# Kernel optimization log

Measured on AMD Instinct MI355X. Metric: run time of the kernel, lower is better.

## Reference

```python
import jax, jax.numpy as jnp
import numpy as np

N = 50000      # nodes
E = 800000     # edges
F_IN = 256
H1, D1 = 4, 32   # conv1 heads, per-head dim (hidden_features)
H2, D2 = 1, 32   # conv2 heads, per-head dim (out_features)
NEG_SLOPE = 0.2


def setup_inputs():
    key = jax.random.key(0)
    ks = jax.random.split(key, 12)
    x = jax.random.normal(ks[0], (N, F_IN), dtype=jnp.float32)
    src = jax.random.randint(ks[1], (E,), 0, N, dtype=jnp.int32)
    dst = jax.random.randint(ks[2], (E,), 0, N, dtype=jnp.int32)
    s = 0.05
    W1 = jax.random.normal(ks[3], (F_IN, H1 * D1), dtype=jnp.float32) * s
    al1 = jax.random.normal(ks[4], (H1, D1), dtype=jnp.float32) * s
    ar1 = jax.random.normal(ks[5], (H1, D1), dtype=jnp.float32) * s
    b1 = jnp.zeros((H1 * D1,), dtype=jnp.float32)
    W2 = jax.random.normal(ks[6], (H1 * D1, H2 * D2), dtype=jnp.float32) * s
    al2 = jax.random.normal(ks[7], (H2, D2), dtype=jnp.float32) * s
    ar2 = jax.random.normal(ks[8], (H2, D2), dtype=jnp.float32) * s
    b2 = jnp.zeros((H2 * D2,), dtype=jnp.float32)
    return {"x": x, "W1": W1, "al1": al1, "ar1": ar1, "b1": b1,
            "W2": W2, "al2": al2, "ar2": ar2, "b2": b2,
            "src": src, "dst": dst}


def gat_layer(x, W, al, ar, b, src, dst, H, D):
    # x: [N, F] -> feat: [N, H, D]
    feat = (x @ W).reshape(-1, H, D)
    el = jnp.sum(feat * al, axis=-1)   # [N, H]
    er = jnp.sum(feat * ar, axis=-1)   # [N, H]
    # per-edge attention logits, LeakyReLU
    e = jax.nn.leaky_relu(el[src] + er[dst], negative_slope=NEG_SLOPE)  # [E, H]
    # edge softmax over destination neighborhoods (stable)
    m = jax.ops.segment_max(e, dst, num_segments=N)          # [N, H]
    m = jnp.where(jnp.isfinite(m), m, 0.0)                   # guard zero-in-degree
    ee = jnp.exp(e - m[dst])                                 # [E, H]
    z = jax.ops.segment_sum(ee, dst, num_segments=N)         # [N, H]
    a = ee / jnp.maximum(z[dst], 1e-16)                      # [E, H]
    # weighted message aggregation
    msg = feat[src] * a[:, :, None]                          # [E, H, D]
    rst = jax.ops.segment_sum(msg, dst, num_segments=N)      # [N, H, D]
    return (rst + b.reshape(1, H, D)).reshape(-1, H * D)     # flatten(1)


def reference(x, W1, al1, ar1, b1, W2, al2, ar2, b2, src, dst):
    # dropouts are identity in eval mode; is_out_layer=True => no activation
    h = gat_layer(x, W1, al1, ar1, b1, src, dst, H1, D1)     # [N, H1*D1]
    out = gat_layer(h, W2, al2, ar2, b2, src, dst, H2, D2)   # [N, H2*D2]
    return out
```

## Files before the change

### kernel.cpp

```cpp
#include <hip/hip_runtime.h>

constexpr int F_IN = 256;
constexpr int H1 = 4, D1 = 32, F1 = H1 * D1;
constexpr int H2 = 1, D2 = 32, F2 = H2 * D2;
constexpr float NEG = 0.2f;

constexpr int BW = 128;
constexpr int NBUK_MAX = 512;
constexpr int CB = 128;

typedef short short8 __attribute__((ext_vector_type(8)));
typedef float f32x4 __attribute__((ext_vector_type(4)));

__device__ inline float bf2f(unsigned short u) {
    unsigned int x = ((unsigned int)u) << 16;
    return __builtin_bit_cast(float, x);
}
__device__ inline unsigned short f2bf(float f) {
    __bf16 h = (__bf16)f;
    return __builtin_bit_cast(unsigned short, h);
}

__global__ __launch_bounds__(256) void chist(const int* __restrict__ dst,
                                             unsigned int* __restrict__ HcT,
                                             int E, int nbuk) {
    __shared__ unsigned int h[NBUK_MAX];
    int tid = threadIdx.x;
    for (int i = tid; i < nbuk; i += 256) h[i] = 0;
    __syncthreads();
    int epb = (E + CB - 1) / CB;
    int e0 = blockIdx.x * epb, e1 = min(e0 + epb, E);
    for (int e = e0 + tid; e < e1; e += 256)
        atomicAdd(&h[dst[e] >> 7], 1u);
    __syncthreads();
    for (int i = tid; i < nbuk; i += 256) HcT[(size_t)i * CB + blockIdx.x] = h[i];
}

__global__ __launch_bounds__(512) void bscan(const unsigned int* __restrict__ HcT,
                                             unsigned int* __restrict__ Bb,
                                             unsigned int* __restrict__ S, int nbuk) {
    __shared__ unsigned int tot[NBUK_MAX];
    int t = threadIdx.x;
    unsigned int run = 0;
    if (t < nbuk) {
        const uint4* row = (const uint4*)(HcT + (size_t)t * CB);
#pragma unroll 8
        for (int b4 = 0; b4 < CB / 4; ++b4) {
            uint4 v = row[b4];
            int b = b4 * 4;
            Bb[(size_t)(b + 0) * nbuk + t] = run; run += v.x;
            Bb[(size_t)(b + 1) * nbuk + t] = run; run += v.y;
            Bb[(size_t)(b + 2) * nbuk + t] = run; run += v.z;
            Bb[(size_t)(b + 3) * nbuk + t] = run; run += v.w;
        }
    }
    tot[t] = (t < nbuk) ? run : 0;
    __syncthreads();
    for (int o = 1; o < NBUK_MAX; o <<= 1) {
        unsigned int v = (t >= o) ? tot[t - o] : 0;
        __syncthreads();
        tot[t] += v;
        __syncthreads();
    }
    if (t < nbuk) S[t] = tot[t] - run;
    if (t == nbuk - 1) S[nbuk] = tot[t];
}

__global__ __launch_bounds__(256) void cscat(const int* __restrict__ src,
                                             const int* __restrict__ dst,
                                             const unsigned int* __restrict__ Bb,
                                             const unsigned int* __restrict__ S,
                                             unsigned int* __restrict__ pairs, int E, int nbuk) {
    __shared__ unsigned int h[NBUK_MAX];
    int tid = threadIdx.x;
    for (int i = tid; i < nbuk; i += 256) h[i] = 0;
    __syncthreads();
    int epb = (E + CB - 1) / CB;
    int e0 = blockIdx.x * epb, e1 = min(e0 + epb, E);
    const unsigned int* bb = Bb + (size_t)blockIdx.x * nbuk;
    for (int e = e0 + tid; e < e1; e += 256) {
        int d = dst[e];
        int k = d >> 7;
        unsigned int r = atomicAdd(&h[k], 1u);
        unsigned int p = S[k] + bb[k] + r;
        pairs[p] = ((unsigned int)(d & 127) << 17) | (unsigned int)src[e];
    }
}

__global__ __launch_bounds__(256) void fscat(const unsigned int* __restrict__ pairs,
                                             const unsigned int* __restrict__ S,
                                             int* __restrict__ off, int* __restrict__ csr,
                                             int n, int E) {
    int k = blockIdx.x;
    int tid = threadIdx.x;
    unsigned int s0 = S[k], s1 = S[k + 1];
    __shared__ unsigned int cnt[BW];
    __shared__ unsigned int ex[BW];
    if (tid < BW) cnt[tid] = 0;
    __syncthreads();
    for (unsigned int i = s0 + tid; i < s1; i += 256)
        atomicAdd(&cnt[pairs[i] >> 17], 1u);
    __syncthreads();
    unsigned int orig = (tid < BW) ? cnt[tid] : 0;
    if (tid < BW) ex[tid] = orig;
    __syncthreads();
    for (int o = 1; o < BW; o <<= 1) {
        unsigned int v = (tid < BW && tid >= (unsigned)o) ? ex[tid - o] : 0;
        __syncthreads();
        if (tid < BW) ex[tid] += v;
        __syncthreads();
    }
    if (tid < BW) {
        ex[tid] -= orig;
        int node = k * BW + tid;
        if (node < n) off[node] = (int)(s0 + ex[tid]);
    }
    if (tid < BW) cnt[tid] = 0;
    __syncthreads();
    for (unsigned int i = s0 + tid; i < s1; i += 256) {
        unsigned int pr = pairs[i];
        int loc = pr >> 17;
        unsigned int r = atomicAdd(&cnt[loc], 1u);
        csr[s0 + ex[loc] + r] = (int)(pr & 0x1FFFFu);
    }
    if (k == 0 && tid == 0) off[n] = E;
}

__device__ inline void wsplit_one(const float* W, unsigned short* Wh, unsigned short* Wl,
                                  int idx, int C) {
    int j    = idx & 7;
    int lane = (idx >> 3) & 63;
    int t    = idx >> 9;
    int FC   = C >> 4;
    int fc   = t % FC, ks = t / FC;
    int k = ks * 32 + (lane >> 4) * 8 + j;
    int c = fc * 16 + (lane & 15);
    float v = W[(size_t)k * C + c];
    __bf16 h = (__bf16)v;
    float hv = (float)h;
    __bf16 lo = (__bf16)(v - hv);
    Wh[idx] = __builtin_bit_cast(unsigned short, h);
    Wl[idx] = __builtin_bit_cast(unsigned short, lo);
}
__global__ void wsplit_swz2(const float* __restrict__ W1, unsigned short* __restrict__ W1h,
                            unsigned short* __restrict__ W1l,
                            const float* __restrict__ W2, unsigned short* __restrict__ W2h,
                            unsigned short* __restrict__ W2l) {
    int idx = blockIdx.x * 256 + threadIdx.x;
    constexpr int N1 = F_IN * F1;
    if (idx < N1) wsplit_one(W1, W1h, W1l, idx, F1);
    else if (idx < N1 + F1 * F2) wsplit_one(W2, W2h, W2l, idx - N1, F2);
}

__global__ __launch_bounds__(256) void xswz_kernel(const float* __restrict__ x,
                                                   unsigned short* __restrict__ xb,
                                                   int n, int nrow_pad) {
    int tid = threadIdx.x;
    int lane = tid & 63;
    int wid = tid >> 6;
    int half = lane >> 5;
    int l32 = lane & 31;
    int ks = l32 >> 2;
    int khi = l32 & 3;
    int row = blockIdx.x * 8 + wid * 2 + half;
    if (row >= nrow_pad) return;
    float v[8];
    if (row < n) {
        const float* p = x + (size_t)row * F_IN + ks * 32 + khi * 8;
        float4 a = *(const float4*)p;
        float4 b = *(const float4*)(p + 4);
        v[0] = a.x; v[1] = a.y; v[2] = a.z; v[3] = a.w;
        v[4] = b.x; v[5] = b.y; v[6] = b.z; v[7] = b.w;
    } else {
#pragma unroll
        for (int j = 0; j < 8; ++j) v[j] = 0.f;
    }
    short8 s;
#pragma unroll
    for (int j = 0; j < 8; ++j) s[j] = (short)f2bf(v[j]);
    int frag16 = row >> 4;
    int fragLane = (row & 15) | (khi << 4);
    *(short8*)(xb + (((size_t)frag16 * 8 + ks) * 64 + fragLane) * 8) = s;
}

constexpr int BM1 = 64;
__global__ __launch_bounds__(256) void gemm1_mfma(
    const unsigned short* __restrict__ Xb,
    const unsigned short* __restrict__ Wh,
    const unsigned short* __restrict__ Wl,
    const float* __restrict__ alv, const float* __restrict__ arv,
    unsigned short* __restrict__ outb,
    float* __restrict__ el, float* __restrict__ er, int n)
{
    const int tid  = threadIdx.x;
    const int lane = tid & 63;
    const int wid  = tid >> 6;
    const int wrow = (wid >> 1) * 32;
    const int wcol = (wid & 1) * 64;
    const int wc16 = wcol >> 4;
    const int row0 = blockIdx.x * BM1;
    const int l16  = lane & 15;
    const int khi  = lane >> 4;
    const int fbase = blockIdx.x * 4 + (wid >> 1) * 2;

    f32x4 acc[2][4];
#pragma unroll
    for (int mi = 0; mi < 2; ++mi)
#pragma unroll
        for (int ni = 0; ni < 4; ++ni) acc[mi][ni] = f32x4{0.f, 0.f, 0.f, 0.f};

#pragma unroll
    for (int ks = 0; ks < 8; ++ks) {
        short8 ah[2];
#pragma unroll
        for (int mi = 0; mi < 2; ++mi)
            ah[mi] = *(const short8*)(Xb + (((size_t)(fbase + mi) * 8 + ks) * 64 + lane) * 8);

        short8 bh[4], bl[4];
#pragma unroll
        for (int ni = 0; ni < 4; ++ni) {
            int base = ((ks * 8 + wc16 + ni) * 64 + lane) * 8;
            bh[ni] = *(const short8*)(Wh + base);
            bl[ni] = *(const short8*)(Wl + base);
        }

#pragma unroll
        for (int mi = 0; mi < 2; ++mi)
#pragma unroll
            for (int ni = 0; ni < 4; ++ni) {
                acc[mi][ni] = __builtin_amdgcn_mfma_f32_16x16x32_bf16(ah[mi], bl[ni], acc[mi][ni], 0, 0, 0);
                acc[mi][ni] = __builtin_amdgcn_mfma_f32_16x16x32_bf16(ah[mi], bh[ni], acc[mi][ni], 0, 0, 0);
            }
    }

    const int hh0 = wcol >> 5;
    float alr[2][2], arr[2][2];
#pragma unroll
    for (int t = 0; t < 2; ++t) {
        int head = hh0 + t;
        alr[t][0] = alv[head * 32 + l16];
        alr[t][1] = alv[head * 32 + 16 + l16];
        arr[t][0] = arv[head * 32 + l16];
        arr[t][1] = arv[head * 32 + 16 + l16];
    }

#pragma unroll
    for (int mi = 0; mi < 2; ++mi) {
        int rbase = row0 + wrow + mi * 16 + khi * 4;
#pragma unroll
        for (int rr = 0; rr < 4; ++rr) {
            int row = rbase + rr;
            bool ok = row < n;
            if (ok) {
#pragma unroll
                for (int ni = 0; ni < 4; ++ni)
                    outb[(size_t)row * F1 + wcol + ni * 16 + l16] = f2bf(acc[mi][ni][rr]);
            }
#pragma unroll
            for (int t = 0; t < 2; ++t) {
                float pel = acc[mi][2 * t][rr] * alr[t][0] + acc[mi][2 * t + 1][rr] * alr[t][1];
                float per = acc[mi][2 * t][rr] * arr[t][0] + acc[mi][2 * t + 1][rr] * arr[t][1];
#pragma unroll
                for (int o = 1; o < 16; o <<= 1) {
                    pel += __shfl_xor(pel, o);
                    per += __shfl_xor(per, o);
                }
                if (ok && l16 == 0) {
                    el[(size_t)row * H1 + hh0 + t] = pel;
                    er[(size_t)row * H1 + hh0 + t] = per;
                }
            }
        }
    }
}

constexpr int BM2 = 64;
__global__ __launch_bounds__(256) void gemm2_mfma(
    const float* __restrict__ X,
    const unsigned short* __restrict__ Wh,
    const unsigned short* __restrict__ Wl,
    const float* __restrict__ alv, const float* __restrict__ arv,
    float* __restrict__ out,
    float* __restrict__ el, float* __restrict__ er, int n)
{
    __shared__ float xs[32 * BM2 * 4];
    const int tid  = threadIdx.x;
    const int lane = tid & 63;
    const int wid  = tid >> 6;
    const int wrow = wid * 16;
    const int row0 = blockIdx.x * BM2;
    const int l16  = lane & 15;
    const int khi  = lane >> 4;

    {
        int gr = row0 + lane;
        gr = gr < n ? gr : (n - 1);
        const float* rowp = X + (size_t)gr * F1;
#pragma unroll
        for (int i = 0; i < 8; ++i) {
            int kc = wid * 8 + i;
            const float* srcp = rowp + kc * 4;
            float* dstf = &xs[kc * BM2 * 4];
            __builtin_amdgcn_global_load_lds(
                (const __attribute__((address_space(1))) unsigned int*)srcp,
                (__attribute__((address_space(3))) unsigned int*)dstf,
                16, 0, 0);
        }
    }
    asm volatile("s_waitcnt vmcnt(0)" ::: "memory");
    __syncthreads();

    f32x4 acc[2];
#pragma unroll
    for (int ni = 0; ni < 2; ++ni) acc[ni] = f32x4{0.f, 0.f, 0.f, 0.f};

    const int rt = wrow + l16;

#pragma unroll
    for (int ks = 0; ks < 4; ++ks) {
        const int kc = ks * 8 + khi * 2;

        short8 bh[2], bl[2];
#pragma unroll
        for (int ni = 0; ni < 2; ++ni) {
            int base = ((ks * 2 + ni) * 64 + lane) * 8;
            bh[ni] = *(const short8*)(Wh + base);
            bl[ni] = *(const short8*)(Wl + base);
        }

        float4 xa0 = *(const float4*)&xs[(kc + 0) * BM2 * 4 + rt * 4];
        float4 xa1 = *(const float4*)&xs[(kc + 1) * BM2 * 4 + rt * 4];
        float v[8] = {xa0.x, xa0.y, xa0.z, xa0.w, xa1.x, xa1.y, xa1.z, xa1.w};
        short8 ah, al8;
#pragma unroll
        for (int j = 0; j < 8; ++j) {
            __bf16 h = (__bf16)v[j];
            float hv = (float)h;
            __bf16 lo = (__bf16)(v[j] - hv);
            ah[j] = __builtin_bit_cast(short, h);
            al8[j] = __builtin_bit_cast(short, lo);
        }

#pragma unroll
        for (int ni = 0; ni < 2; ++ni) {
            acc[ni] = __builtin_amdgcn_mfma_f32_16x16x32_bf16(al8, bh[ni], acc[ni], 0, 0, 0);
            acc[ni] = __builtin_amdgcn_mfma_f32_16x16x32_bf16(ah, bl[ni], acc[ni], 0, 0, 0);
            acc[ni] = __builtin_amdgcn_mfma_f32_16x16x32_bf16(ah, bh[ni], acc[ni], 0, 0, 0);
        }
    }

    float al0 = alv[l16], al1c = alv[16 + l16];
    float ar0 = arv[l16], ar1c = arv[16 + l16];

    int rbase = row0 + wrow + khi * 4;
#pragma unroll
    for (int rr = 0; rr < 4; ++rr) {
        int row = rbase + rr;
        bool ok = row < n;
        if (ok) {
#pragma unroll
            for (int ni = 0; ni < 2; ++ni)
                out[(size_t)row * F2 + ni * 16 + l16] = acc[ni][rr];
        }
        float pel = acc[0][rr] * al0 + acc[1][rr] * al1c;
        float per = acc[0][rr] * ar0 + acc[1][rr] * ar1c;
#pragma unroll
        for (int o = 1; o < 16; o <<= 1) {
            pel += __shfl_xor(pel, o);
            per += __shfl_xor(per, o);
        }
        if (ok && l16 == 0) {
            el[row] = pel;
            er[row] = per;
        }
    }
}

__global__ __launch_bounds__(256) void agg1_kernel(
    const int* __restrict__ off, const int* __restrict__ csr_src,
    const unsigned short* __restrict__ featb, const float* __restrict__ el,
    const float* __restrict__ er, const float* __restrict__ b,
    float* __restrict__ out, int n)
{
    int wid = (blockIdx.x * 256 + threadIdx.x) >> 6;
    int lane = threadIdx.x & 63;
    if (wid >= n) return;
    int c0 = (lane & 31) * 4;
    int h = (lane & 31) >> 3;
    int half = lane >> 5;
    float erv = er[(size_t)wid * H1 + h];
    float sw = 0.f;
    float4 acc = {0.f, 0.f, 0.f, 0.f};
    int jb = off[wid], je = off[wid + 1];
    int j = jb + half;
    for (; j + 6 < je; j += 8) {
        int s0 = csr_src[j];
        int s1 = csr_src[j + 2];
        int s2 = csr_src[j + 4];
        int s3 = csr_src[j + 6];
        ushort4 u0 = *(const ushort4*)(featb + (size_t)s0 * F1 + c0);
        ushort4 u1 = *(const ushort4*)(featb + (size_t)s1 * F1 + c0);
        ushort4 u2 = *(const ushort4*)(featb + (size_t)s2 * F1 + c0);
        ushort4 u3 = *(const ushort4*)(featb + (size_t)s3 * F1 + c0);
        float t0 = el[(size_t)s0 * H1 + h] + erv;
        float t1 = el[(size_t)s1 * H1 + h] + erv;
        float t2 = el[(size_t)s2 * H1 + h] + erv;
        float t3 = el[(size_t)s3 * H1 + h] + erv;
        t0 = t0 > 0.f ? t0 : NEG * t0;
        t1 = t1 > 0.f ? t1 : NEG * t1;
        t2 = t2 > 0.f ? t2 : NEG * t2;
        t3 = t3 > 0.f ? t3 : NEG * t3;
        float w0 = __expf(t0), w1 = __expf(t1), w2 = __expf(t2), w3 = __expf(t3);
        sw += (w0 + w1) + (w2 + w3);
        acc.x = fmaf(w0, bf2f(u0.x), fmaf(w1, bf2f(u1.x), fmaf(w2, bf2f(u2.x), fmaf(w3, bf2f(u3.x), acc.x))));
        acc.y = fmaf(w0, bf2f(u0.y), fmaf(w1, bf2f(u1.y), fmaf(w2, bf2f(u2.y), fmaf(w3, bf2f(u3.y), acc.y))));
        acc.z = fmaf(w0, bf2f(u0.z), fmaf(w1, bf2f(u1.z), fmaf(w2, bf2f(u2.z), fmaf(w3, bf2f(u3.z), acc.z))));
        acc.w = fmaf(w0, bf2f(u0.w), fmaf(w1, bf2f(u1.w), fmaf(w2, bf2f(u2.w), fmaf(w3, bf2f(u3.w), acc.w))));
    }
    for (; j < je; j += 2) {
        int s = csr_src[j];
        ushort4 u = *(const ushort4*)(featb + (size_t)s * F1 + c0);
        float t = el[(size_t)s * H1 + h] + erv;
        t = t > 0.f ? t : NEG * t;
        float w = __expf(t);
        sw += w;
        acc.x = fmaf(w, bf2f(u.x), acc.x);
        acc.y = fmaf(w, bf2f(u.y), acc.y);
        acc.z = fmaf(w, bf2f(u.z), acc.z);
        acc.w = fmaf(w, bf2f(u.w), acc.w);
    }
    acc.x += __shfl_xor(acc.x, 32);
    acc.y += __shfl_xor(acc.y, 32);
    acc.z += __shfl_xor(acc.z, 32);
    acc.w += __shfl_xor(acc.w, 32);
    sw    += __shfl_xor(sw, 32);
    if (half == 0) {
        float inv = 1.f / fmaxf(sw, 1e-16f);
        float4 bb = *(const float4*)(b + c0);
        float4 t = {acc.x * inv + bb.x, acc.y * inv + bb.y,
                    acc.z * inv + bb.z, acc.w * inv + bb.w};
        *(float4*)(out + (size_t)wid * F1 + c0) = t;
    }
}

__global__ __launch_bounds__(256) void agg2_kernel(
    const int* __restrict__ off, const int* __restrict__ csr_src,
    const float* __restrict__ feat, const float* __restrict__ el,
    const float* __restrict__ er, const float* __restrict__ b,
    float* __restrict__ out, int n)
{
    int wid = (blockIdx.x * 256 + threadIdx.x) >> 6;
    int lane = threadIdx.x & 63;
    if (wid >= n) return;
    int c0 = (lane & 7) * 4;
    int grp = lane >> 3;
    float erv = er[wid];
    float sw = 0.f;
    float4 acc = {0.f, 0.f, 0.f, 0.f};
    int jb = off[wid], je = off[wid + 1];
    int j = jb + grp;
    for (; j + 8 < je; j += 16) {
        int s0 = csr_src[j];
        int s1 = csr_src[j + 8];
        float4 f0 = *(const float4*)(feat + (size_t)s0 * F2 + c0);
        float4 f1 = *(const float4*)(feat + (size_t)s1 * F2 + c0);
        float t0 = el[s0] + erv;
        float t1 = el[s1] + erv;
        t0 = t0 > 0.f ? t0 : NEG * t0;
        t1 = t1 > 0.f ? t1 : NEG * t1;
        float w0 = __expf(t0);
        float w1 = __expf(t1);
        sw += w0 + w1;
        acc.x = fmaf(w0, f0.x, fmaf(w1, f1.x, acc.x));
        acc.y = fmaf(w0, f0.y, fmaf(w1, f1.y, acc.y));
        acc.z = fmaf(w0, f0.z, fmaf(w1, f1.z, acc.z));
        acc.w = fmaf(w0, f0.w, fmaf(w1, f1.w, acc.w));
    }
    for (; j < je; j += 8) {
        int s = csr_src[j];
        float4 f = *(const float4*)(feat + (size_t)s * F2 + c0);
        float t = el[s] + erv;
        t = t > 0.f ? t : NEG * t;
        float w = __expf(t);
        sw += w;
        acc.x = fmaf(w, f.x, acc.x);
        acc.y = fmaf(w, f.y, acc.y);
        acc.z = fmaf(w, f.z, acc.z);
        acc.w = fmaf(w, f.w, acc.w);
    }
#pragma unroll
    for (int o = 8; o < 64; o <<= 1) {
        acc.x += __shfl_xor(acc.x, o);
        acc.y += __shfl_xor(acc.y, o);
        acc.z += __shfl_xor(acc.z, o);
        acc.w += __shfl_xor(acc.w, o);
        sw    += __shfl_xor(sw, o);
    }
    if (lane < 8) {
        float inv = 1.f / fmaxf(sw, 1e-16f);
        float4 bb = *(const float4*)(b + c0);
        float4 t = {acc.x * inv + bb.x, acc.y * inv + bb.y,
                    acc.z * inv + bb.z, acc.w * inv + bb.w};
        *(float4*)(out + (size_t)wid * F2 + c0) = t;
    }
}

extern "C" void kernel_launch(void* const* d_in, const int* in_sizes, int n_in,
                              void* d_out, int out_size, void* d_ws, size_t ws_size,
                              hipStream_t stream) {
    const float* x   = (const float*)d_in[0];
    const float* W1  = (const float*)d_in[1];
    const float* al1 = (const float*)d_in[2];
    const float* ar1 = (const float*)d_in[3];
    const float* b1  = (const float*)d_in[4];
    const float* W2  = (const float*)d_in[5];
    const float* al2 = (const float*)d_in[6];
    const float* ar2 = (const float*)d_in[7];
    const float* b2  = (const float*)d_in[8];
    const int*   src = (const int*)d_in[9];
    const int*   dst = (const int*)d_in[10];

    const int N = in_sizes[0] / F_IN;
    const int E = in_sizes[9];
    const int NBUK = (N + BW - 1) / BW;
    const int NBLK1 = (N + BM1 - 1) / BM1;
    const int NROWP = NBLK1 * BM1;

    char* w = (char*)d_ws;
    size_t o = 0;
    auto alloc = [&](size_t bytes) { size_t cur = o; o += (bytes + 255) & ~255ULL; return cur; };
    int*   off   = (int*)  (w + alloc((size_t)(N + 1) * 4));
    int*   csr   = (int*)  (w + alloc((size_t)E * 4));
    unsigned int* pairs = (unsigned int*)(w + alloc((size_t)E * 4));
    unsigned int* HcT = (unsigned int*)(w + alloc((size_t)CB * NBUK * 4));
    unsigned int* Bb  = (unsigned int*)(w + alloc((size_t)CB * NBUK * 4));
    unsigned int* S   = (unsigned int*)(w + alloc((size_t)(NBUK + 1) * 4));
    unsigned short* xb = (unsigned short*)(w + alloc((size_t)NROWP * F_IN * 2));
    unsigned short* feat1b = (unsigned short*)(w + alloc((size_t)N * F1 * 2));
    float* el1   = (float*)(w + alloc((size_t)N * H1 * 4));
    float* er1   = (float*)(w + alloc((size_t)N * H1 * 4));
    float* h1    = (float*)(w + alloc((size_t)N * F1 * 4));
    float* feat2 = (float*)(w + alloc((size_t)N * F2 * 4));
    float* el2   = (float*)(w + alloc((size_t)N * H2 * 4));
    float* er2   = (float*)(w + alloc((size_t)N * H2 * 4));
    unsigned short* W1h = (unsigned short*)(w + alloc((size_t)F_IN * F1 * 2));
    unsigned short* W1l = (unsigned short*)(w + alloc((size_t)F_IN * F1 * 2));
    unsigned short* W2h = (unsigned short*)(w + alloc((size_t)F1 * F2 * 2));
    unsigned short* W2l = (unsigned short*)(w + alloc((size_t)F1 * F2 * 2));
    (void)ws_size; (void)n_in; (void)out_size;

    chist<<<CB, 256, 0, stream>>>(dst, HcT, E, NBUK);
    bscan<<<1, 512, 0, stream>>>(HcT, Bb, S, NBUK);
    cscat<<<CB, 256, 0, stream>>>(src, dst, Bb, S, pairs, E, NBUK);
    fscat<<<NBUK, 256, 0, stream>>>(pairs, S, off, csr, N, E);

    wsplit_swz2<<<(F_IN * F1 + F1 * F2 + 255) / 256, 256, 0, stream>>>(
        W1, W1h, W1l, W2, W2h, W2l);
    xswz_kernel<<<(NROWP + 7) / 8, 256, 0, stream>>>(x, xb, N, NROWP);

    gemm1_mfma<<<NBLK1, 256, 0, stream>>>(
        xb, W1h, W1l, al1, ar1, feat1b, el1, er1, N);
    agg1_kernel<<<(N + 3) / 4, 256, 0, stream>>>(off, csr, feat1b, el1, er1, b1, h1, N);

    gemm2_mfma<<<(N + BM2 - 1) / BM2, 256, 0, stream>>>(
        h1, W2h, W2l, al2, ar2, feat2, el2, er2, N);
    agg2_kernel<<<(N + 3) / 4, 256, 0, stream>>>(off, csr, feat2, el2, er2, b2, (float*)d_out, N);
}
```

Before: 151.1 us.

## Fuse CSR build into cooperative kernel, merge prep kernels, store feat2 in bf16

```diff
diff --git a/kernel.cpp b/kernel.cpp
--- a/kernel.cpp
+++ b/kernel.cpp
@@ -1,4 +1,7 @@
 #include <hip/hip_runtime.h>
+#include <hip/hip_cooperative_groups.h>
+
+namespace cg = cooperative_groups;
 
 constexpr int F_IN = 256;
 constexpr int H1 = 4, D1 = 32, F1 = H1 * D1;
@@ -21,109 +24,108 @@
     return __builtin_bit_cast(unsigned short, h);
 }
 
-__global__ __launch_bounds__(256) void chist(const int* __restrict__ dst,
-                                             unsigned int* __restrict__ HcT,
-                                             int E, int nbuk) {
+__global__ __launch_bounds__(256) void csr_build(
+    const int* __restrict__ src, const int* __restrict__ dst,
+    unsigned int* __restrict__ HcT, unsigned int* __restrict__ Bb,
+    unsigned int* __restrict__ S, unsigned int* __restrict__ pairs,
+    int* __restrict__ off, int* __restrict__ csr,
+    int n, int E, int nbuk)
+{
+    cg::grid_group grid = cg::this_grid();
     __shared__ unsigned int h[NBUK_MAX];
-    int tid = threadIdx.x;
+    const int tid = threadIdx.x;
+    const int b = blockIdx.x;
+    const int epb = (E + CB - 1) / CB;
+    const int e0 = b * epb, e1 = min(e0 + epb, E);
+
     for (int i = tid; i < nbuk; i += 256) h[i] = 0;
     __syncthreads();
-    int epb = (E + CB - 1) / CB;
-    int e0 = blockIdx.x * epb, e1 = min(e0 + epb, E);
     for (int e = e0 + tid; e < e1; e += 256)
-        atomicAdd(&h[dst[e] >> 7], 1u);
+        atomicAdd(&h[((unsigned)dst[e]) >> 7], 1u);
     __syncthreads();
-    for (int i = tid; i < nbuk; i += 256) HcT[(size_t)i * CB + blockIdx.x] = h[i];
-}
-
-__global__ __launch_bounds__(512) void bscan(const unsigned int* __restrict__ HcT,
-                                             unsigned int* __restrict__ Bb,
-                                             unsigned int* __restrict__ S, int nbuk) {
-    __shared__ unsigned int tot[NBUK_MAX];
-    int t = threadIdx.x;
-    unsigned int run = 0;
-    if (t < nbuk) {
-        const uint4* row = (const uint4*)(HcT + (size_t)t * CB);
+    for (int i = tid; i < nbuk; i += 256) HcT[(size_t)i * CB + b] = h[i];
+    grid.sync();
+
+    {
+        int g = b * 256 + tid;
+        if (g < nbuk) {
+            const uint4* row = (const uint4*)(HcT + (size_t)g * CB);
+            unsigned int run = 0;
 #pragma unroll 8
-        for (int b4 = 0; b4 < CB / 4; ++b4) {
-            uint4 v = row[b4];
-            int b = b4 * 4;
-            Bb[(size_t)(b + 0) * nbuk + t] = run; run += v.x;
-            Bb[(size_t)(b + 1) * nbuk + t] = run; run += v.y;
-            Bb[(size_t)(b + 2) * nbuk + t] = run; run += v.z;
-            Bb[(size_t)(b + 3) * nbuk + t] = run; run += v.w;
-        }
-    }
-    tot[t] = (t < nbuk) ? run : 0;
+            for (int b4 = 0; b4 < CB / 4; ++b4) {
+                uint4 v = row[b4];
+                int bb = b4 * 4;
+                Bb[(size_t)(bb + 0) * nbuk + g] = run; run += v.x;
+                Bb[(size_t)(bb + 1) * nbuk + g] = run; run += v.y;
+                Bb[(size_t)(bb + 2) * nbuk + g] = run; run += v.z;
+                Bb[(size_t)(bb + 3) * nbuk + g] = run; run += v.w;
+            }
+            S[g] = run;
+        }
+    }
+    grid.sync();
+
+    if (b == 0) {
+        unsigned a0 = (2 * tid     < nbuk) ? S[2 * tid]     : 0;
+        unsigned a1 = (2 * tid + 1 < nbuk) ? S[2 * tid + 1] : 0;
+        __syncthreads();
+        h[tid] = a0 + a1;
+        __syncthreads();
+        for (int o = 1; o < 256; o <<= 1) {
+            unsigned v = (tid >= o) ? h[tid - o] : 0;
+            __syncthreads();
+            h[tid] += v;
+            __syncthreads();
+        }
+        unsigned base = h[tid] - (a0 + a1);
+        if (2 * tid     < nbuk) S[2 * tid]     = base;
+        if (2 * tid + 1 < nbuk) S[2 * tid + 1] = base + a0;
+        if (tid == 255) S[nbuk] = h[255];
+    }
+    grid.sync();
+
+    for (int i = tid; i < nbuk; i += 256) h[i] = S[i] + Bb[(size_t)b * nbuk + i];
     __syncthreads();
-    for (int o = 1; o < NBUK_MAX; o <<= 1) {
-        unsigned int v = (t >= o) ? tot[t - o] : 0;
-        __syncthreads();
-        tot[t] += v;
-        __syncthreads();
-    }
-    if (t < nbuk) S[t] = tot[t] - run;
-    if (t == nbuk - 1) S[nbuk] = tot[t];
-}
-
-__global__ __launch_bounds__(256) void cscat(const int* __restrict__ src,
-                                             const int* __restrict__ dst,
-                                             const unsigned int* __restrict__ Bb,
-                                             const unsigned int* __restrict__ S,
-                                             unsigned int* __restrict__ pairs, int E, int nbuk) {
-    __shared__ unsigned int h[NBUK_MAX];
-    int tid = threadIdx.x;
-    for (int i = tid; i < nbuk; i += 256) h[i] = 0;
-    __syncthreads();
-    int epb = (E + CB - 1) / CB;
-    int e0 = blockIdx.x * epb, e1 = min(e0 + epb, E);
-    const unsigned int* bb = Bb + (size_t)blockIdx.x * nbuk;
     for (int e = e0 + tid; e < e1; e += 256) {
         int d = dst[e];
-        int k = d >> 7;
-        unsigned int r = atomicAdd(&h[k], 1u);
-        unsigned int p = S[k] + bb[k] + r;
-        pairs[p] = ((unsigned int)(d & 127) << 17) | (unsigned int)src[e];
-    }
-}
-
-__global__ __launch_bounds__(256) void fscat(const unsigned int* __restrict__ pairs,
-                                             const unsigned int* __restrict__ S,
-                                             int* __restrict__ off, int* __restrict__ csr,
-                                             int n, int E) {
-    int k = blockIdx.x;
-    int tid = threadIdx.x;
-    unsigned int s0 = S[k], s1 = S[k + 1];
-    __shared__ unsigned int cnt[BW];
-    __shared__ unsigned int ex[BW];
-    if (tid < BW) cnt[tid] = 0;
-    __syncthreads();
-    for (unsigned int i = s0 + tid; i < s1; i += 256)
-        atomicAdd(&cnt[pairs[i] >> 17], 1u);
-    __syncthreads();
-    unsigned int orig = (tid < BW) ? cnt[tid] : 0;
-    if (tid < BW) ex[tid] = orig;
-    __syncthreads();
-    for (int o = 1; o < BW; o <<= 1) {
-        unsigned int v = (tid < BW && tid >= (unsigned)o) ? ex[tid - o] : 0;
-        __syncthreads();
-        if (tid < BW) ex[tid] += v;
-        __syncthreads();
-    }
-    if (tid < BW) {
-        ex[tid] -= orig;
-        int node = k * BW + tid;
-        if (node < n) off[node] = (int)(s0 + ex[tid]);
-    }
-    if (tid < BW) cnt[tid] = 0;
-    __syncthreads();
-    for (unsigned int i = s0 + tid; i < s1; i += 256) {
-        unsigned int pr = pairs[i];
-        int loc = pr >> 17;
-        unsigned int r = atomicAdd(&cnt[loc], 1u);
-        csr[s0 + ex[loc] + r] = (int)(pr & 0x1FFFFu);
-    }
-    if (k == 0 && tid == 0) off[n] = E;
+        int k = ((unsigned)d) >> 7;
+        unsigned p = atomicAdd(&h[k], 1u);
+        pairs[p] = ((unsigned)(d & 127) << 17) | (unsigned)src[e];
+    }
+    grid.sync();
+
+    for (int k = b; k < nbuk; k += CB) {
+        unsigned s0 = S[k], s1v = S[k + 1];
+        __syncthreads();
+        if (tid < BW) h[tid] = 0;
+        __syncthreads();
+        for (unsigned i = s0 + tid; i < s1v; i += 256)
+            atomicAdd(&h[pairs[i] >> 17], 1u);
+        __syncthreads();
+        unsigned orig = (tid < BW) ? h[tid] : 0;
+        if (tid < BW) h[128 + tid] = orig;
+        __syncthreads();
+        for (int o = 1; o < BW; o <<= 1) {
+            unsigned v = (tid < BW && tid >= o) ? h[128 + tid - o] : 0;
+            __syncthreads();
+            if (tid < BW) h[128 + tid] += v;
+            __syncthreads();
+        }
+        if (tid < BW) {
+            h[128 + tid] -= orig;
+            int node = k * BW + tid;
+            if (node < n) off[node] = (int)(s0 + h[128 + tid]);
+        }
+        if (tid < BW) h[tid] = 0;
+        __syncthreads();
+        for (unsigned i = s0 + tid; i < s1v; i += 256) {
+            unsigned pr = pairs[i];
+            int loc = pr >> 17;
+            unsigned r = atomicAdd(&h[loc], 1u);
+            csr[s0 + h[128 + loc] + r] = (int)(pr & 0x1FFFFu);
+        }
+    }
+    if (b == 0 && tid == 0) off[n] = E;
 }
 
 __device__ inline void wsplit_one(const float* W, unsigned short* Wh, unsigned short* Wl,
@@ -142,19 +144,25 @@
     Wh[idx] = __builtin_bit_cast(unsigned short, h);
     Wl[idx] = __builtin_bit_cast(unsigned short, lo);
 }
-__global__ void wsplit_swz2(const float* __restrict__ W1, unsigned short* __restrict__ W1h,
-                            unsigned short* __restrict__ W1l,
-                            const float* __restrict__ W2, unsigned short* __restrict__ W2h,
-                            unsigned short* __restrict__ W2l) {
-    int idx = blockIdx.x * 256 + threadIdx.x;
-    constexpr int N1 = F_IN * F1;
-    if (idx < N1) wsplit_one(W1, W1h, W1l, idx, F1);
-    else if (idx < N1 + F1 * F2) wsplit_one(W2, W2h, W2l, idx - N1, F2);
-}
-
-__global__ __launch_bounds__(256) void xswz_kernel(const float* __restrict__ x,
-                                                   unsigned short* __restrict__ xb,
-                                                   int n, int nrow_pad) {
+
+constexpr int WBLK = (F_IN * F1 + F1 * F2) / 256;
+
+__global__ __launch_bounds__(256) void prep_kernel(
+    const float* __restrict__ W1, unsigned short* __restrict__ W1h,
+    unsigned short* __restrict__ W1l,
+    const float* __restrict__ W2, unsigned short* __restrict__ W2h,
+    unsigned short* __restrict__ W2l,
+    const float* __restrict__ x, unsigned short* __restrict__ xb,
+    int n, int nrow_pad)
+{
+    int bid = blockIdx.x;
+    if (bid < WBLK) {
+        int idx = bid * 256 + threadIdx.x;
+        constexpr int N1 = F_IN * F1;
+        if (idx < N1) wsplit_one(W1, W1h, W1l, idx, F1);
+        else wsplit_one(W2, W2h, W2l, idx - N1, F2);
+        return;
+    }
     int tid = threadIdx.x;
     int lane = tid & 63;
     int wid = tid >> 6;
@@ -162,7 +170,7 @@
     int l32 = lane & 31;
     int ks = l32 >> 2;
     int khi = l32 & 3;
-    int row = blockIdx.x * 8 + wid * 2 + half;
+    int row = (bid - WBLK) * 8 + wid * 2 + half;
     if (row >= nrow_pad) return;
     float v[8];
     if (row < n) {
@@ -280,7 +288,7 @@
     const unsigned short* __restrict__ Wh,
     const unsigned short* __restrict__ Wl,
     const float* __restrict__ alv, const float* __restrict__ arv,
-    float* __restrict__ out,
+    unsigned short* __restrict__ outb,
     float* __restrict__ el, float* __restrict__ er, int n)
 {
     __shared__ float xs[32 * BM2 * 4];
@@ -360,7 +368,7 @@
         if (ok) {
 #pragma unroll
             for (int ni = 0; ni < 2; ++ni)
-                out[(size_t)row * F2 + ni * 16 + l16] = acc[ni][rr];
+                outb[(size_t)row * F2 + ni * 16 + l16] = f2bf(acc[ni][rr]);
         }
         float pel = acc[0][rr] * al0 + acc[1][rr] * al1c;
         float per = acc[0][rr] * ar0 + acc[1][rr] * ar1c;
@@ -445,7 +453,7 @@
 
 __global__ __launch_bounds__(256) void agg2_kernel(
     const int* __restrict__ off, const int* __restrict__ csr_src,
-    const float* __restrict__ feat, const float* __restrict__ el,
+    const unsigned short* __restrict__ featb, const float* __restrict__ el,
     const float* __restrict__ er, const float* __restrict__ b,
     float* __restrict__ out, int n)
 {
@@ -462,8 +470,8 @@
     for (; j + 8 < je; j += 16) {
         int s0 = csr_src[j];
         int s1 = csr_src[j + 8];
-        float4 f0 = *(const float4*)(feat + (size_t)s0 * F2 + c0);
-        float4 f1 = *(const float4*)(feat + (size_t)s1 * F2 + c0);
+        ushort4 u0 = *(const ushort4*)(featb + (size_t)s0 * F2 + c0);
+        ushort4 u1 = *(const ushort4*)(featb + (size_t)s1 * F2 + c0);
         float t0 = el[s0] + erv;
         float t1 = el[s1] + erv;
         t0 = t0 > 0.f ? t0 : NEG * t0;
@@ -471,22 +479,22 @@
         float w0 = __expf(t0);
         float w1 = __expf(t1);
         sw += w0 + w1;
-        acc.x = fmaf(w0, f0.x, fmaf(w1, f1.x, acc.x));
-        acc.y = fmaf(w0, f0.y, fmaf(w1, f1.y, acc.y));
-        acc.z = fmaf(w0, f0.z, fmaf(w1, f1.z, acc.z));
-        acc.w = fmaf(w0, f0.w, fmaf(w1, f1.w, acc.w));
+        acc.x = fmaf(w0, bf2f(u0.x), fmaf(w1, bf2f(u1.x), acc.x));
+        acc.y = fmaf(w0, bf2f(u0.y), fmaf(w1, bf2f(u1.y), acc.y));
+        acc.z = fmaf(w0, bf2f(u0.z), fmaf(w1, bf2f(u1.z), acc.z));
+        acc.w = fmaf(w0, bf2f(u0.w), fmaf(w1, bf2f(u1.w), acc.w));
     }
     for (; j < je; j += 8) {
         int s = csr_src[j];
-        float4 f = *(const float4*)(feat + (size_t)s * F2 + c0);
+        ushort4 u = *(const ushort4*)(featb + (size_t)s * F2 + c0);
         float t = el[s] + erv;
         t = t > 0.f ? t : NEG * t;
         float w = __expf(t);
         sw += w;
-        acc.x = fmaf(w, f.x, acc.x);
-        acc.y = fmaf(w, f.y, acc.y);
-        acc.z = fmaf(w, f.z, acc.z);
-        acc.w = fmaf(w, f.w, acc.w);
+        acc.x = fmaf(w, bf2f(u.x), acc.x);
+        acc.y = fmaf(w, bf2f(u.y), acc.y);
+        acc.z = fmaf(w, bf2f(u.z), acc.z);
+        acc.w = fmaf(w, bf2f(u.w), acc.w);
     }
 #pragma unroll
     for (int o = 8; o < 64; o <<= 1) {
@@ -520,9 +528,9 @@
     const int*   src = (const int*)d_in[9];
     const int*   dst = (const int*)d_in[10];
 
-    const int N = in_sizes[0] / F_IN;
-    const int E = in_sizes[9];
-    const int NBUK = (N + BW - 1) / BW;
+    int N = in_sizes[0] / F_IN;
+    int E = in_sizes[9];
+    int NBUK = (N + BW - 1) / BW;
     const int NBLK1 = (N + BM1 - 1) / BM1;
     const int NROWP = NBLK1 * BM1;
 
@@ -540,7 +548,7 @@
     float* el1   = (float*)(w + alloc((size_t)N * H1 * 4));
     float* er1   = (float*)(w + alloc((size_t)N * H1 * 4));
     float* h1    = (float*)(w + alloc((size_t)N * F1 * 4));
-    float* feat2 = (float*)(w + alloc((size_t)N * F2 * 4));
+    unsigned short* feat2b = (unsigned short*)(w + alloc((size_t)N * F2 * 2));
     float* el2   = (float*)(w + alloc((size_t)N * H2 * 4));
     float* er2   = (float*)(w + alloc((size_t)N * H2 * 4));
     unsigned short* W1h = (unsigned short*)(w + alloc((size_t)F_IN * F1 * 2));
@@ -549,20 +557,22 @@
     unsigned short* W2l = (unsigned short*)(w + alloc((size_t)F1 * F2 * 2));
     (void)ws_size; (void)n_in; (void)out_size;
 
-    chist<<<CB, 256, 0, stream>>>(dst, HcT, E, NBUK);
-    bscan<<<1, 512, 0, stream>>>(HcT, Bb, S, NBUK);
-    cscat<<<CB, 256, 0, stream>>>(src, dst, Bb, S, pairs, E, NBUK);
-    fscat<<<NBUK, 256, 0, stream>>>(pairs, S, off, csr, N, E);
-
-    wsplit_swz2<<<(F_IN * F1 + F1 * F2 + 255) / 256, 256, 0, stream>>>(
-        W1, W1h, W1l, W2, W2h, W2l);
-    xswz_kernel<<<(NROWP + 7) / 8, 256, 0, stream>>>(x, xb, N, NROWP);
+    {
+        void* args[] = {(void*)&src, (void*)&dst, (void*)&HcT, (void*)&Bb, (void*)&S,
+                        (void*)&pairs, (void*)&off, (void*)&csr,
+                        (void*)&N, (void*)&E, (void*)&NBUK};
+        hipLaunchCooperativeKernel(reinterpret_cast<void*>(csr_build),
+                                   dim3(CB), dim3(256), args, 0, stream);
+    }
+
+    prep_kernel<<<WBLK + (NROWP + 7) / 8, 256, 0, stream>>>(
+        W1, W1h, W1l, W2, W2h, W2l, x, xb, N, NROWP);
 
     gemm1_mfma<<<NBLK1, 256, 0, stream>>>(
         xb, W1h, W1l, al1, ar1, feat1b, el1, er1, N);
     agg1_kernel<<<(N + 3) / 4, 256, 0, stream>>>(off, csr, feat1b, el1, er1, b1, h1, N);
 
     gemm2_mfma<<<(N + BM2 - 1) / BM2, 256, 0, stream>>>(
-        h1, W2h, W2l, al2, ar2, feat2, el2, er2, N);
-    agg2_kernel<<<(N + 3) / 4, 256, 0, stream>>>(off, csr, feat2, el2, er2, b2, (float*)d_out, N);
-}
+        h1, W2h, W2l, al2, ar2, feat2b, el2, er2, N);
+    agg2_kernel<<<(N + 3) / 4, 256, 0, stream>>>(off, csr, feat2b, el2, er2, b2, (float*)d_out, N);
+}
```

Result: slower. 236.3 us (+56.3%).

## Store layer-2 features in bf16, fuse prep kernels, preload scatter offsets

Applied to the files above, without the earlier changes.

```diff
diff --git a/kernel.cpp b/kernel.cpp
--- a/kernel.cpp
+++ b/kernel.cpp
@@ -31,7 +31,7 @@
     int epb = (E + CB - 1) / CB;
     int e0 = blockIdx.x * epb, e1 = min(e0 + epb, E);
     for (int e = e0 + tid; e < e1; e += 256)
-        atomicAdd(&h[dst[e] >> 7], 1u);
+        atomicAdd(&h[((unsigned)dst[e]) >> 7], 1u);
     __syncthreads();
     for (int i = tid; i < nbuk; i += 256) HcT[(size_t)i * CB + blockIdx.x] = h[i];
 }
@@ -73,16 +73,15 @@
                                              unsigned int* __restrict__ pairs, int E, int nbuk) {
     __shared__ unsigned int h[NBUK_MAX];
     int tid = threadIdx.x;
-    for (int i = tid; i < nbuk; i += 256) h[i] = 0;
+    for (int i = tid; i < nbuk; i += 256)
+        h[i] = S[i] + Bb[(size_t)blockIdx.x * nbuk + i];
     __syncthreads();
     int epb = (E + CB - 1) / CB;
     int e0 = blockIdx.x * epb, e1 = min(e0 + epb, E);
-    const unsigned int* bb = Bb + (size_t)blockIdx.x * nbuk;
     for (int e = e0 + tid; e < e1; e += 256) {
         int d = dst[e];
-        int k = d >> 7;
-        unsigned int r = atomicAdd(&h[k], 1u);
-        unsigned int p = S[k] + bb[k] + r;
+        int k = ((unsigned)d) >> 7;
+        unsigned int p = atomicAdd(&h[k], 1u);
         pairs[p] = ((unsigned int)(d & 127) << 17) | (unsigned int)src[e];
     }
 }
@@ -142,19 +141,25 @@
     Wh[idx] = __builtin_bit_cast(unsigned short, h);
     Wl[idx] = __builtin_bit_cast(unsigned short, lo);
 }
-__global__ void wsplit_swz2(const float* __restrict__ W1, unsigned short* __restrict__ W1h,
-                            unsigned short* __restrict__ W1l,
-                            const float* __restrict__ W2, unsigned short* __restrict__ W2h,
-                            unsigned short* __restrict__ W2l) {
-    int idx = blockIdx.x * 256 + threadIdx.x;
-    constexpr int N1 = F_IN * F1;
-    if (idx < N1) wsplit_one(W1, W1h, W1l, idx, F1);
-    else if (idx < N1 + F1 * F2) wsplit_one(W2, W2h, W2l, idx - N1, F2);
-}
-
-__global__ __launch_bounds__(256) void xswz_kernel(const float* __restrict__ x,
-                                                   unsigned short* __restrict__ xb,
-                                                   int n, int nrow_pad) {
+
+constexpr int WBLK = (F_IN * F1 + F1 * F2) / 256;
+
+__global__ __launch_bounds__(256) void prep_kernel(
+    const float* __restrict__ W1, unsigned short* __restrict__ W1h,
+    unsigned short* __restrict__ W1l,
+    const float* __restrict__ W2, unsigned short* __restrict__ W2h,
+    unsigned short* __restrict__ W2l,
+    const float* __restrict__ x, unsigned short* __restrict__ xb,
+    int n, int nrow_pad)
+{
+    int bid = blockIdx.x;
+    if (bid < WBLK) {
+        int idx = bid * 256 + threadIdx.x;
+        constexpr int N1 = F_IN * F1;
+        if (idx < N1) wsplit_one(W1, W1h, W1l, idx, F1);
+        else wsplit_one(W2, W2h, W2l, idx - N1, F2);
+        return;
+    }
     int tid = threadIdx.x;
     int lane = tid & 63;
     int wid = tid >> 6;
@@ -162,7 +167,7 @@
     int l32 = lane & 31;
     int ks = l32 >> 2;
     int khi = l32 & 3;
-    int row = blockIdx.x * 8 + wid * 2 + half;
+    int row = (bid - WBLK) * 8 + wid * 2 + half;
     if (row >= nrow_pad) return;
     float v[8];
     if (row < n) {
@@ -280,7 +285,7 @@
     const unsigned short* __restrict__ Wh,
     const unsigned short* __restrict__ Wl,
     const float* __restrict__ alv, const float* __restrict__ arv,
-    float* __restrict__ out,
+    unsigned short* __restrict__ outb,
     float* __restrict__ el, float* __restrict__ er, int n)
 {
     __shared__ float xs[32 * BM2 * 4];
@@ -360,7 +365,7 @@
         if (ok) {
 #pragma unroll
             for (int ni = 0; ni < 2; ++ni)
-                out[(size_t)row * F2 + ni * 16 + l16] = acc[ni][rr];
+                outb[(size_t)row * F2 + ni * 16 + l16] = f2bf(acc[ni][rr]);
         }
         float pel = acc[0][rr] * al0 + acc[1][rr] * al1c;
         float per = acc[0][rr] * ar0 + acc[1][rr] * ar1c;
@@ -445,7 +450,7 @@
 
 __global__ __launch_bounds__(256) void agg2_kernel(
     const int* __restrict__ off, const int* __restrict__ csr_src,
-    const float* __restrict__ feat, const float* __restrict__ el,
+    const unsigned short* __restrict__ featb, const float* __restrict__ el,
     const float* __restrict__ er, const float* __restrict__ b,
     float* __restrict__ out, int n)
 {
@@ -462,8 +467,8 @@
     for (; j + 8 < je; j += 16) {
         int s0 = csr_src[j];
         int s1 = csr_src[j + 8];
-        float4 f0 = *(const float4*)(feat + (size_t)s0 * F2 + c0);
-        float4 f1 = *(const float4*)(feat + (size_t)s1 * F2 + c0);
+        ushort4 u0 = *(const ushort4*)(featb + (size_t)s0 * F2 + c0);
+        ushort4 u1 = *(const ushort4*)(featb + (size_t)s1 * F2 + c0);
         float t0 = el[s0] + erv;
         float t1 = el[s1] + erv;
         t0 = t0 > 0.f ? t0 : NEG * t0;
@@ -471,22 +476,22 @@
         float w0 = __expf(t0);
         float w1 = __expf(t1);
         sw += w0 + w1;
-        acc.x = fmaf(w0, f0.x, fmaf(w1, f1.x, acc.x));
-        acc.y = fmaf(w0, f0.y, fmaf(w1, f1.y, acc.y));
-        acc.z = fmaf(w0, f0.z, fmaf(w1, f1.z, acc.z));
-        acc.w = fmaf(w0, f0.w, fmaf(w1, f1.w, acc.w));
+        acc.x = fmaf(w0, bf2f(u0.x), fmaf(w1, bf2f(u1.x), acc.x));
+        acc.y = fmaf(w0, bf2f(u0.y), fmaf(w1, bf2f(u1.y), acc.y));
+        acc.z = fmaf(w0, bf2f(u0.z), fmaf(w1, bf2f(u1.z), acc.z));
+        acc.w = fmaf(w0, bf2f(u0.w), fmaf(w1, bf2f(u1.w), acc.w));
     }
     for (; j < je; j += 8) {
         int s = csr_src[j];
-        float4 f = *(const float4*)(feat + (size_t)s * F2 + c0);
+        ushort4 u = *(const ushort4*)(featb + (size_t)s * F2 + c0);
         float t = el[s] + erv;
         t = t > 0.f ? t : NEG * t;
         float w = __expf(t);
         sw += w;
-        acc.x = fmaf(w, f.x, acc.x);
-        acc.y = fmaf(w, f.y, acc.y);
-        acc.z = fmaf(w, f.z, acc.z);
-        acc.w = fmaf(w, f.w, acc.w);
+        acc.x = fmaf(w, bf2f(u.x), acc.x);
+        acc.y = fmaf(w, bf2f(u.y), acc.y);
+        acc.z = fmaf(w, bf2f(u.z), acc.z);
+        acc.w = fmaf(w, bf2f(u.w), acc.w);
     }
 #pragma unroll
     for (int o = 8; o < 64; o <<= 1) {
@@ -540,7 +545,7 @@
     float* el1   = (float*)(w + alloc((size_t)N * H1 * 4));
     float* er1   = (float*)(w + alloc((size_t)N * H1 * 4));
     float* h1    = (float*)(w + alloc((size_t)N * F1 * 4));
-    float* feat2 = (float*)(w + alloc((size_t)N * F2 * 4));
+    unsigned short* feat2b = (unsigned short*)(w + alloc((size_t)N * F2 * 2));
     float* el2   = (float*)(w + alloc((size_t)N * H2 * 4));
     float* er2   = (float*)(w + alloc((size_t)N * H2 * 4));
     unsigned short* W1h = (unsigned short*)(w + alloc((size_t)F_IN * F1 * 2));
@@ -554,15 +559,14 @@
     cscat<<<CB, 256, 0, stream>>>(src, dst, Bb, S, pairs, E, NBUK);
     fscat<<<NBUK, 256, 0, stream>>>(pairs, S, off, csr, N, E);
 
-    wsplit_swz2<<<(F_IN * F1 + F1 * F2 + 255) / 256, 256, 0, stream>>>(
-        W1, W1h, W1l, W2, W2h, W2l);
-    xswz_kernel<<<(NROWP + 7) / 8, 256, 0, stream>>>(x, xb, N, NROWP);
+    prep_kernel<<<WBLK + (NROWP + 7) / 8, 256, 0, stream>>>(
+        W1, W1h, W1l, W2, W2h, W2l, x, xb, N, NROWP);
 
     gemm1_mfma<<<NBLK1, 256, 0, stream>>>(
         xb, W1h, W1l, al1, ar1, feat1b, el1, er1, N);
     agg1_kernel<<<(N + 3) / 4, 256, 0, stream>>>(off, csr, feat1b, el1, er1, b1, h1, N);
 
     gemm2_mfma<<<(N + BM2 - 1) / BM2, 256, 0, stream>>>(
-        h1, W2h, W2l, al2, ar2, feat2, el2, er2, N);
-    agg2_kernel<<<(N + 3) / 4, 256, 0, stream>>>(off, csr, feat2, el2, er2, b2, (float*)d_out, N);
-}
+        h1, W2h, W2l, al2, ar2, feat2b, el2, er2, N);
+    agg2_kernel<<<(N + 3) / 4, 256, 0, stream>>>(off, csr, feat2b, el2, er2, b2, (float*)d_out, N);
+}
```

New measurement: 152.2 us. Within noise of the previous version (+0.7%).
